# Performance work log

Measured on AMD Instinct MI355X. Metric: run time of the kernel, lower is better.

Reference implementation:

```python
import jax, jax.numpy as jnp
import numpy as np

N = 50000
D_IN = 512
D_OUT = 512
NUM_SAMPLE = 2


def setup_inputs() -> dict:
    key = jax.random.key(0)
    ks = jax.random.split(key, 8)
    x = jax.random.normal(ks[0], (N, D_IN), dtype=jnp.float32)
    neighs1 = jax.random.randint(ks[1], (N, NUM_SAMPLE), 0, N, dtype=jnp.int32)
    neighs2 = jax.random.randint(ks[2], (N, NUM_SAMPLE), 0, N, dtype=jnp.int32)
    # SageLayer weights: [out, 2*in] (self || aggregated neighbors), xavier-ish scale
    W1 = jax.random.normal(ks[3], (D_OUT, 2 * D_IN), dtype=jnp.float32) * 0.03
    W2 = jax.random.normal(ks[4], (D_OUT, 2 * D_OUT), dtype=jnp.float32) * 0.03
    fc_w = jax.random.normal(ks[5], (2, N * D_OUT), dtype=jnp.float32) * 0.0005
    fc_b = jnp.zeros((2,), dtype=jnp.float32)
    return {"x": x, "neighs1": neighs1, "neighs2": neighs2,
            "W1": W1, "W2": W2, "fc_w": fc_w, "fc_b": fc_b}


def _sage_layer(h, neighs, W):
    # MEAN aggregation over the num_sample sampled neighbors (self excluded, gcn=False).
    # Equivalent to the original dense one-hot mask.div(num_neigh).mm(embed_matrix).
    agg = h[neighs].mean(axis=1)                      # [N, S, d] -> [N, d]
    combined = jnp.concatenate([h, agg], axis=1)      # [N, 2d]
    # F.relu(W.mm(combined.t())).t() == relu(combined @ W.T)
    return jax.nn.relu(combined @ W.T)                # [N, out]


def reference(x, neighs1, neighs2, W1, W2, fc_w, fc_b):
    h = _sage_layer(x, neighs1, W1)
    h = _sage_layer(h, neighs2, W2)
    flat = h.reshape(1, -1)                           # [1, N*out]
    logits = flat @ fc_w.T + fc_b                     # [1, 2]
    return (flat, jax.nn.log_softmax(logits, axis=1))
```

## Files before the change

### kernel.cpp

```cpp
#include <hip/hip_runtime.h>
#include <stdint.h>

typedef short bf16x8 __attribute__((ext_vector_type(8)));
typedef float f32x4 __attribute__((ext_vector_type(4)));
typedef unsigned short u16x8 __attribute__((ext_vector_type(8)));

#define N_NODES 50000
#define DIM 512
#define KDIM 1024
#define NPAD 50048
#define M_TILES 391
#define GEMM_GRID 3136
#define FLAT_TOTAL 25600000ULL
#define NBLK_AGG 12500

__device__ __forceinline__ unsigned short f2bf(float f) {
    unsigned u = __float_as_uint(f);
    unsigned r = u + 0x7FFFu + ((u >> 16) & 1u);
    return (unsigned short)(r >> 16);
}
__device__ __forceinline__ float bf2f(unsigned short h) {
    return __uint_as_float(((unsigned)h) << 16);
}

__device__ __forceinline__ void llds16(const void* g, void* l) {
    __builtin_amdgcn_global_load_lds(
        (const __attribute__((address_space(1))) void*)g,
        (__attribute__((address_space(3))) void*)l,
        16, 0, 0);
}

__global__ void cast_x(const float* __restrict__ x, unsigned short* __restrict__ XA) {
    size_t idx = ((size_t)blockIdx.x * blockDim.x + threadIdx.x) * 8;
    float4 v0 = *(const float4*)&x[idx];
    float4 v1 = *(const float4*)&x[idx + 4];
    u16x8 r;
    r[0] = f2bf(v0.x); r[1] = f2bf(v0.y); r[2] = f2bf(v0.z); r[3] = f2bf(v0.w);
    r[4] = f2bf(v1.x); r[5] = f2bf(v1.y); r[6] = f2bf(v1.z); r[7] = f2bf(v1.w);
    size_t row = idx >> 9;
    size_t col = idx & 511;
    *(u16x8*)&XA[row * KDIM + col] = r;
}

__global__ void cast_w2(const float* __restrict__ w1, const float* __restrict__ w2,
                        unsigned short* __restrict__ o1, unsigned short* __restrict__ o2) {
    int b = blockIdx.x;
    const float* w = (b < 256) ? w1 : w2;
    unsigned short* o = (b < 256) ? o1 : o2;
    int idx = ((b & 255) * 256 + threadIdx.x) * 8;
    float4 v0 = *(const float4*)&w[idx];
    float4 v1 = *(const float4*)&w[idx + 4];
    u16x8 r;
    r[0] = f2bf(v0.x); r[1] = f2bf(v0.y); r[2] = f2bf(v0.z); r[3] = f2bf(v0.w);
    r[4] = f2bf(v1.x); r[5] = f2bf(v1.y); r[6] = f2bf(v1.z); r[7] = f2bf(v1.w);
    *(u16x8*)&o[idx] = r;
}

__global__ void agg_mean(unsigned short* __restrict__ buf, const int* __restrict__ nb) {
    int t = threadIdx.x;
    int i = blockIdx.x * 4 + (t >> 6);
    int lane = t & 63;
    int c = lane * 8;
    int n0 = nb[i * 2], n1 = nb[i * 2 + 1];
    u16x8 a = *(const u16x8*)&buf[(size_t)n0 * KDIM + c];
    u16x8 b = *(const u16x8*)&buf[(size_t)n1 * KDIM + c];
    u16x8 o;
#pragma unroll
    for (int j = 0; j < 8; j++)
        o[j] = f2bf(0.5f * (bf2f(a[j]) + bf2f(b[j])));
    *(u16x8*)&buf[(size_t)i * KDIM + 512 + c] = o;
}


#define SYNC0() do { \
    asm volatile("s_waitcnt vmcnt(0) lgkmcnt(0)" ::: "memory"); \
    __builtin_amdgcn_sched_barrier(0); \
    __builtin_amdgcn_s_barrier(); \
    __builtin_amdgcn_sched_barrier(0); \
} while (0)

#define STAGE(s, ks) do { \
    int koff_ = (ks) * 32; \
    llds16(ga + koff_,            &S[s][t * 8]); \
    llds16(ga + koff_ + 64*KDIM,  &S[s][2048 + t * 8]); \
    llds16(gb + koff_,            &S[s][4096 + t * 8]); \
} while (0)

#define COMPUTE(s) do { \
    bf16x8 af[4], bfr[2]; \
    _Pragma("unroll") \
    for (int i_ = 0; i_ < 4; i_++) af[i_] = *(const bf16x8*)&S[s][aoff[i_]]; \
    _Pragma("unroll") \
    for (int j_ = 0; j_ < 2; j_++) bfr[j_] = *(const bf16x8*)&S[s][boff[j_]]; \
    _Pragma("unroll") \
    for (int i_ = 0; i_ < 4; i_++) \
        _Pragma("unroll") \
        for (int j_ = 0; j_ < 2; j_++) \
            acc[i_][j_] = __builtin_amdgcn_mfma_f32_16x16x32_bf16(af[i_], bfr[j_], acc[i_][j_], 0, 0, 0); \
} while (0)

template <int EPI>
__global__ __launch_bounds__(256, 6)
void gemm_nt(const unsigned short* __restrict__ A, const unsigned short* __restrict__ B,
             unsigned short* __restrict__ H, const float* __restrict__ fcw,
             float* __restrict__ out, float2* __restrict__ partials) {
    __shared__ unsigned short S[2][6144];
    __shared__ float r0[4], r1[4];

    int x = blockIdx.x & 7;
    int g = blockIdx.x >> 3;
    int bm = x + 8 * (g >> 3);
    int bn = g & 7;
    if (bm >= M_TILES) {
        if (EPI == 2 && threadIdx.x == 0) partials[blockIdx.x] = make_float2(0.f, 0.f);
        return;
    }

    int t = threadIdx.x;
    int lane = t & 63;
    int wave = t >> 6;
    int m_off = (wave >> 1) * 64;
    int n_off = (wave & 1) * 32;
    int lrow = lane & 15;
    int lch = lane >> 4;

    f32x4 acc[4][2];
#pragma unroll
    for (int i = 0; i < 4; i++)
#pragma unroll
        for (int j = 0; j < 2; j++) acc[i][j] = (f32x4){0.f, 0.f, 0.f, 0.f};

    int aoff[4], boff[2];
#pragma unroll
    for (int i = 0; i < 4; i++) {
        int r = m_off + i * 16 + lrow;
        aoff[i] = r * 32 + ((lch ^ ((r >> 1) & 3)) * 8);
    }
#pragma unroll
    for (int j = 0; j < 2; j++) {
        int r = n_off + j * 16 + lrow;
        boff[j] = 4096 + r * 32 + ((lch ^ ((r >> 1) & 3)) * 8);
    }

    int trow = t >> 2;
    int tchk = ((t & 3) ^ ((t >> 3) & 3)) * 8;
    const unsigned short* ga = A + (size_t)(bm * 128 + trow) * KDIM + tchk;
    const unsigned short* gb = B + (size_t)(bn * 64 + trow) * KDIM + tchk;

    STAGE(0, 0);
    SYNC0();
#pragma unroll 1
    for (int ks = 0; ks < 32; ks += 2) {
        STAGE(1, ks + 1);
        COMPUTE(0);
        SYNC0();
        if (ks + 2 < 32) STAGE(0, ks + 2);
        COMPUTE(1);
        SYNC0();
    }

    int lc = lane & 15;
    int lr = (lane >> 4) << 2;

    if (EPI == 1) {
#pragma unroll
        for (int i = 0; i < 4; i++) {
            int row0 = bm * 128 + m_off + i * 16 + lr;
#pragma unroll
            for (int j = 0; j < 2; j++) {
                int col = bn * 64 + n_off + j * 16 + lc;
                f32x4 v = acc[i][j];
#pragma unroll
                for (int r = 0; r < 4; r++)
                    H[(size_t)(row0 + r) * KDIM + col] = f2bf(fmaxf(v[r], 0.f));
            }
        }
    } else {
        float s0 = 0.f, s1 = 0.f;
#pragma unroll
        for (int i = 0; i < 4; i++) {
            int row0 = bm * 128 + m_off + i * 16 + lr;
#pragma unroll
            for (int j = 0; j < 2; j++) {
                int col = bn * 64 + n_off + j * 16 + lc;
                f32x4 v = acc[i][j];
#pragma unroll
                for (int r = 0; r < 4; r++) {
                    int row = row0 + r;
                    if (row < N_NODES) {
                        float vv = fmaxf(v[r], 0.f);
                        size_t off = (size_t)row * DIM + col;
                        out[off] = vv;
                        s0 += vv * fcw[off];
                        s1 += vv * fcw[FLAT_TOTAL + off];
                    }
                }
            }
        }
#pragma unroll
        for (int off = 32; off > 0; off >>= 1) {
            s0 += __shfl_down(s0, off);
            s1 += __shfl_down(s1, off);
        }
        if (lane == 0) { r0[wave] = s0; r1[wave] = s1; }
        __syncthreads();
        if (t == 0)
            partials[blockIdx.x] = make_float2(r0[0] + r0[1] + r0[2] + r0[3],
                                               r1[0] + r1[1] + r1[2] + r1[3]);
    }
}

__global__ void reduce_finalize(const float2* __restrict__ partials, const float* __restrict__ fcb,
                                float* __restrict__ out2) {
    float s0 = 0.f, s1 = 0.f;
    for (int k = threadIdx.x; k < GEMM_GRID; k += 1024) {
        float2 pr = partials[k];
        s0 += pr.x; s1 += pr.y;
    }
#pragma unroll
    for (int off = 32; off > 0; off >>= 1) {
        s0 += __shfl_down(s0, off);
        s1 += __shfl_down(s1, off);
    }
    __shared__ float r0[16], r1[16];
    int lane = threadIdx.x & 63, w = threadIdx.x >> 6;
    if (lane == 0) { r0[w] = s0; r1[w] = s1; }
    __syncthreads();
    if (threadIdx.x == 0) {
        float l0 = fcb[0], l1 = fcb[1];
#pragma unroll
        for (int k = 0; k < 16; k++) { l0 += r0[k]; l1 += r1[k]; }
        float m = fmaxf(l0, l1);
        float lse = m + logf(expf(l0 - m) + expf(l1 - m));
        out2[0] = l0 - lse;
        out2[1] = l1 - lse;
    }
}

extern "C" void kernel_launch(void* const* d_in, const int* in_sizes, int n_in,
                              void* d_out, int out_size, void* d_ws, size_t ws_size,
                              hipStream_t stream) {
    const float* x   = (const float*)d_in[0];
    const int*   n1  = (const int*)d_in[1];
    const int*   n2  = (const int*)d_in[2];
    const float* W1  = (const float*)d_in[3];
    const float* W2  = (const float*)d_in[4];
    const float* fcw = (const float*)d_in[5];
    const float* fcb = (const float*)d_in[6];
    float* out = (float*)d_out;

    char* ws = (char*)d_ws;
    const size_t XA_OFF = 0;
    const size_t HA_OFF = XA_OFF + (size_t)NPAD * KDIM * 2;
    const size_t W1_OFF = HA_OFF + (size_t)NPAD * KDIM * 2;
    const size_t W2_OFF = W1_OFF + (size_t)DIM * KDIM * 2;
    const size_t P_OFF  = W2_OFF + (size_t)DIM * KDIM * 2;
    unsigned short* XA  = (unsigned short*)(ws + XA_OFF);
    unsigned short* HA  = (unsigned short*)(ws + HA_OFF);
    unsigned short* W1r = (unsigned short*)(ws + W1_OFF);
    unsigned short* W2r = (unsigned short*)(ws + W2_OFF);
    float2* partials    = (float2*)(ws + P_OFF);

    cast_w2<<<512, 256, 0, stream>>>(W1, W2, W1r, W2r);
    cast_x<<<12500, 256, 0, stream>>>(x, XA);

    agg_mean<<<NBLK_AGG, 256, 0, stream>>>(XA, n1);
    gemm_nt<1><<<GEMM_GRID, 256, 0, stream>>>(XA, W1r, HA, nullptr, nullptr, nullptr);
    agg_mean<<<NBLK_AGG, 256, 0, stream>>>(HA, n2);
    gemm_nt<2><<<GEMM_GRID, 256, 0, stream>>>(HA, W2r, nullptr, fcw, out, partials);

    reduce_finalize<<<1, 1024, 0, stream>>>(partials, fcb, out + FLAT_TOTAL);
}
```

Baseline: 627.7 us.

## Deepen GEMM LDS pipeline to four stages and stage epilogue through LDS

The K-loop moves from a double-buffered LDS scheme with a full vmcnt(0) wait per step to a four-buffer ring that waits only for the oldest outstanding loads. This lets global-to-LDS loads run further ahead of the MFMAs, and s_setprio is raised around the MFMA block. Both epilogues now write the tile into LDS first and then issue coalesced 16-byte stores plus vectorized fc_w loads, replacing scattered 2- and 4-byte accesses. The larger LDS footprint lowers the occupancy target from 6 to 3 blocks per CU.

Result: faster. 589.2 us (-6.1%).

```diff
diff --git a/kernel.cpp b/kernel.cpp
--- a/kernel.cpp
+++ b/kernel.cpp
@@ -72,39 +72,49 @@
 }
 
 
-#define SYNC0() do { \
-    asm volatile("s_waitcnt vmcnt(0) lgkmcnt(0)" ::: "memory"); \
-    __builtin_amdgcn_sched_barrier(0); \
-    __builtin_amdgcn_s_barrier(); \
-    __builtin_amdgcn_sched_barrier(0); \
+#define SB4 6144
+
+#define STAGE(b, ks) do { \
+    int koff_ = (ks) * 32; \
+    llds16(ga + koff_,            &S[(b) * SB4 + t * 8]); \
+    llds16(ga + koff_ + 64*KDIM,  &S[(b) * SB4 + 2048 + t * 8]); \
+    llds16(gb + koff_,            &S[(b) * SB4 + 4096 + t * 8]); \
 } while (0)
 
-#define STAGE(s, ks) do { \
-    int koff_ = (ks) * 32; \
-    llds16(ga + koff_,            &S[s][t * 8]); \
-    llds16(ga + koff_ + 64*KDIM,  &S[s][2048 + t * 8]); \
-    llds16(gb + koff_,            &S[s][4096 + t * 8]); \
-} while (0)
-
-#define COMPUTE(s) do { \
+#define COMPUTE(b) do { \
     bf16x8 af[4], bfr[2]; \
     _Pragma("unroll") \
-    for (int i_ = 0; i_ < 4; i_++) af[i_] = *(const bf16x8*)&S[s][aoff[i_]]; \
+    for (int i_ = 0; i_ < 4; i_++) af[i_] = *(const bf16x8*)&S[(b) * SB4 + aoff[i_]]; \
     _Pragma("unroll") \
-    for (int j_ = 0; j_ < 2; j_++) bfr[j_] = *(const bf16x8*)&S[s][boff[j_]]; \
+    for (int j_ = 0; j_ < 2; j_++) bfr[j_] = *(const bf16x8*)&S[(b) * SB4 + boff[j_]]; \
+    __builtin_amdgcn_s_setprio(1); \
     _Pragma("unroll") \
     for (int i_ = 0; i_ < 4; i_++) \
         _Pragma("unroll") \
         for (int j_ = 0; j_ < 2; j_++) \
             acc[i_][j_] = __builtin_amdgcn_mfma_f32_16x16x32_bf16(af[i_], bfr[j_], acc[i_][j_], 0, 0, 0); \
+    __builtin_amdgcn_s_setprio(0); \
 } while (0)
 
+#define WAITBAR(vm) do { \
+    asm volatile("s_waitcnt vmcnt(" #vm ") lgkmcnt(0)" ::: "memory"); \
+    __builtin_amdgcn_sched_barrier(0); \
+    __builtin_amdgcn_s_barrier(); \
+    __builtin_amdgcn_sched_barrier(0); \
+} while (0)
+
+#define STEP(cb, sb, ks_) do { \
+    WAITBAR(3); \
+    STAGE(sb, ks_); \
+    COMPUTE(cb); \
+} while (0)
+
 template <int EPI>
-__global__ __launch_bounds__(256, 6)
+__global__ __launch_bounds__(256, 3)
 void gemm_nt(const unsigned short* __restrict__ A, const unsigned short* __restrict__ B,
              unsigned short* __restrict__ H, const float* __restrict__ fcw,
              float* __restrict__ out, float2* __restrict__ partials) {
-    __shared__ unsigned short S[2][6144];
+    __shared__ unsigned short S[4 * SB4];
     __shared__ float r0[4], r1[4];
 
     int x = blockIdx.x & 7;
@@ -148,53 +158,78 @@
     const unsigned short* gb = B + (size_t)(bn * 64 + trow) * KDIM + tchk;
 
     STAGE(0, 0);
-    SYNC0();
+    STAGE(1, 1);
+
 #pragma unroll 1
-    for (int ks = 0; ks < 32; ks += 2) {
-        STAGE(1, ks + 1);
-        COMPUTE(0);
-        SYNC0();
-        if (ks + 2 < 32) STAGE(0, ks + 2);
-        COMPUTE(1);
-        SYNC0();
-    }
+    for (int trip = 0; trip < 7; trip++) {
+        int ks = trip * 4;
+        STEP(0, 2, ks + 2);
+        STEP(1, 3, ks + 3);
+        STEP(2, 0, ks + 4);
+        STEP(3, 1, ks + 5);
+    }
+    STEP(0, 2, 30);
+    STEP(1, 3, 31);
+    WAITBAR(3);  COMPUTE(2);
+    WAITBAR(0);  COMPUTE(3);
+
+    asm volatile("s_waitcnt lgkmcnt(0)" ::: "memory");
+    __builtin_amdgcn_sched_barrier(0);
+    __builtin_amdgcn_s_barrier();
+    __builtin_amdgcn_sched_barrier(0);
 
     int lc = lane & 15;
     int lr = (lane >> 4) << 2;
 
     if (EPI == 1) {
-#pragma unroll
-        for (int i = 0; i < 4; i++) {
-            int row0 = bm * 128 + m_off + i * 16 + lr;
+        unsigned short* Ct = S;
+#pragma unroll
+        for (int i = 0; i < 4; i++)
 #pragma unroll
             for (int j = 0; j < 2; j++) {
-                int col = bn * 64 + n_off + j * 16 + lc;
                 f32x4 v = acc[i][j];
 #pragma unroll
                 for (int r = 0; r < 4; r++)
-                    H[(size_t)(row0 + r) * KDIM + col] = f2bf(fmaxf(v[r], 0.f));
+                    Ct[(m_off + i * 16 + lr + r) * 72 + n_off + j * 16 + lc] =
+                        f2bf(fmaxf(v[r], 0.f));
             }
+        __syncthreads();
+#pragma unroll
+        for (int it = 0; it < 4; it++) {
+            int ci = it * 256 + t;
+            int row = ci >> 3;
+            int ch = (ci & 7) * 8;
+            u16x8 v = *(const u16x8*)&Ct[row * 72 + ch];
+            *(u16x8*)&H[(size_t)(bm * 128 + row) * KDIM + bn * 64 + ch] = v;
         }
     } else {
+        float* Cf = (float*)S;
+#pragma unroll
+        for (int i = 0; i < 4; i++)
+#pragma unroll
+            for (int j = 0; j < 2; j++) {
+                f32x4 v = acc[i][j];
+#pragma unroll
+                for (int r = 0; r < 4; r++)
+                    Cf[(m_off + i * 16 + lr + r) * 72 + n_off + j * 16 + lc] =
+                        fmaxf(v[r], 0.f);
+            }
+        __syncthreads();
         float s0 = 0.f, s1 = 0.f;
 #pragma unroll
-        for (int i = 0; i < 4; i++) {
-            int row0 = bm * 128 + m_off + i * 16 + lr;
-#pragma unroll
-            for (int j = 0; j < 2; j++) {
-                int col = bn * 64 + n_off + j * 16 + lc;
-                f32x4 v = acc[i][j];
-#pragma unroll
-                for (int r = 0; r < 4; r++) {
-                    int row = row0 + r;
-                    if (row < N_NODES) {
-                        float vv = fmaxf(v[r], 0.f);
-                        size_t off = (size_t)row * DIM + col;
-                        out[off] = vv;
-                        s0 += vv * fcw[off];
-                        s1 += vv * fcw[FLAT_TOTAL + off];
-                    }
-                }
+        for (int it = 0; it < 8; it++) {
+            int ci = it * 256 + t;
+            int row = ci >> 4;
+            int ch = (ci & 15) * 4;
+            int grow = bm * 128 + row;
+            if (grow < N_NODES) {
+                float4 v = *(const float4*)&Cf[row * 72 + ch];
+                size_t off = (size_t)grow * DIM + bn * 64 + ch;
+                *(float4*)&out[off] = v;
+                float4 a = *(const float4*)&fcw[off];
+                float4 b = *(const float4*)&fcw[FLAT_TOTAL + off];
+                s0 += v.x * a.x + v.y * a.y + v.z * a.z + v.w * a.w;
+                s1 += v.x * b.x + v.y * b.y + v.z * b.z + v.w * b.w;
             }
         }
 #pragma unroll
```
